# Performance work log

Hardware: AMD Instinct MI355X
Metric: run time of the kernel (lower is better)

Reference implementation:

```python
import jax, jax.numpy as jnp
import numpy as np

B, N, D_ROI = 16, 128, 12544   # images, detections/image, C*roi*roi = 256*7*7
HID, PARTS = 128, 22
DTH, CTH = 50.0, 0.8           # dist / cosine thresholds
EPS = 1e-12


def setup_inputs() -> dict:
    key = jax.random.key(0)
    ks = jax.random.split(key, 6)
    d_in = D_ROI + 2
    fv = jax.random.normal(ks[0], (B, N, D_ROI), jnp.float32)
    ctr = jax.random.uniform(ks[1], (B, N, 2), jnp.float32) * 640.0  # xyxyn*640 centers
    W1 = jax.random.normal(ks[2], (d_in, HID), jnp.float32) / np.float32(np.sqrt(d_in))
    b1 = jnp.zeros((HID,), jnp.float32)
    W2 = jax.random.normal(ks[3], (HID, HID), jnp.float32) / np.float32(np.sqrt(HID))
    b2 = jnp.zeros((HID,), jnp.float32)
    Wc = jax.random.normal(ks[4], (HID, PARTS), jnp.float32) / np.float32(np.sqrt(HID))
    bc = jnp.zeros((PARTS,), jnp.float32)
    return {"fv": fv, "ctr": ctr, "W1": W1, "b1": b1, "W2": W2, "b2": b2, "Wc": Wc, "bc": bc}


def _adjacency(fv, ctr):
    """Per-image graph build: (cdist < dth) | (cosine > cth), + PyG self-loop."""
    # squared pairwise distance (compare against DTH^2; avoids sqrt at 0)
    d2 = jnp.sum((ctr[:, :, None, :] - ctr[:, None, :, :]) ** 2, axis=-1)  # [B,N,N]
    fvn = fv / jnp.maximum(jnp.linalg.norm(fv, axis=-1, keepdims=True), EPS)
    cos = jnp.einsum("bnd,bmd->bnm", fvn, fvn)                              # [B,N,N]
    A = ((d2 < DTH * DTH) | (cos > CTH)).astype(jnp.float32)
    # GCNConv(add_self_loops=True) adds weight-1 self loops on top of existing edges
    A = A + jnp.eye(N, dtype=jnp.float32)
    deg = jnp.sum(A, axis=-1)                                               # >= 2 on diag
    dinv = jax.lax.rsqrt(deg)
    return dinv[:, :, None] * A * dinv[:, None, :]                          # D^-1/2 A D^-1/2


def reference(fv, ctr, W1, b1, W2, b2, Wc, bc):
    A_hat = _adjacency(fv, ctr)                         # [B,N,N]
    x = jnp.concatenate([fv, ctr], axis=-1)             # [B,N,D_roi+2]
    h = jax.nn.relu(jnp.einsum("bnm,bmh->bnh", A_hat, x @ W1) + b1)
    h = jax.nn.relu(jnp.einsum("bnm,bmh->bnh", A_hat, h @ W2) + b2)
    hg = jnp.mean(h, axis=1)                            # global_mean_pool per image
    logits = hg @ Wc + bc                               # [B, PARTS]
    return logits
```

## Files before the change

kernel.cpp:

```cpp
#include <hip/hip_runtime.h>
#include <stdint.h>

#define DROI   12544
#define BIMG   16
#define NDET   128
#define NHID   128

typedef __bf16 bf16x8 __attribute__((ext_vector_type(8)));
typedef float  f32x4  __attribute__((ext_vector_type(4)));

__device__ __forceinline__ unsigned pk2(float a, float b){
  unsigned ua = __float_as_uint(a), ub = __float_as_uint(b);
  ua = (ua + 0x7fffu + ((ua >> 16) & 1u)) >> 16;
  ub = (ub + 0x7fffu + ((ub >> 16) & 1u)) >> 16;
  return ua | (ub << 16);
}
__device__ __forceinline__ unsigned short bf1(float a){
  unsigned ua = __float_as_uint(a);
  return (unsigned short)((ua + 0x7fffu + ((ua >> 16) & 1u)) >> 16);
}
__device__ __forceinline__ f32x4 mfma16(bf16x8 a, bf16x8 b, f32x4 c){
  return __builtin_amdgcn_mfma_f32_16x16x32_bf16(a, b, c, 0, 0, 0);
}
__device__ __forceinline__ void gl_lds16(const void* g, void* l){
  __builtin_amdgcn_global_load_lds(
      (const __attribute__((address_space(1))) unsigned int*)g,
      (__attribute__((address_space(3))) unsigned int*)l, 16, 0, 0);
}
__device__ __forceinline__ bf16x8 ldfrag128(const short* base, int row, int bo){
  const char* p = (const char*)base + row * 128 + (bo ^ ((row & 7) << 4));
  return *(const bf16x8*)p;
}
__device__ __forceinline__ bf16x8 ldfrag256(const short* base, int row, int bo){
  const char* p = (const char*)base + row * 256 + (bo ^ ((row & 7) << 4));
  return *(const bf16x8*)p;
}

__global__ __launch_bounds__(256) void k0_wt(const float* __restrict__ W1,
                                             unsigned short* __restrict__ Wt){
  __shared__ float tile[64][133];
  const int t  = threadIdx.x;
  const int k0 = blockIdx.x * 64;
  const int r0 = t >> 5;
  const int c4 = (t & 31) * 4;
#pragma unroll
  for (int i = 0; i < 8; ++i){
    int r = r0 + i * 8;
    float4 v = *(const float4*)(W1 + (long)(k0 + r) * NHID + c4);
    tile[r][c4+0] = v.x; tile[r][c4+1] = v.y; tile[r][c4+2] = v.z; tile[r][c4+3] = v.w;
  }
  __syncthreads();
  const int h  = t >> 1;
  const int kc = (t & 1) * 32;
  unsigned* dst = (unsigned*)(Wt + (long)h * DROI + k0 + kc);
#pragma unroll
  for (int kk = 0; kk < 32; kk += 2)
    dst[kk >> 1] = pk2(tile[kc + kk][h], tile[kc + kk + 1][h]);
}

template<int SK>
__global__ __launch_bounds__(512, 4) void k1_main(const float* __restrict__ fv,
    const unsigned short* __restrict__ Wt, unsigned* __restrict__ part){
  constexpr int KC = DROI / SK;
  constexpr int NT = KC / 64;
  static_assert(NT >= 3, "pipeline needs >=3 tiles");
  __shared__ __align__(16) short lsA[2][8192];
  __shared__ __align__(16) short lsB[3][8192];
  const int tid  = threadIdx.x;
  const int wave = tid >> 6, lane = tid & 63;

  const int nwg  = SK * BIMG;
  const int cpx  = nwg >> 3;
  const int orig = blockIdx.x;
  const int wg   = (orig & 7) * cpx + (orig >> 3);
  const int s = wg >> 4;
  const int b = wg & 15;
  const int kbase = s * KC;

  f32x4 acc[2][8];
  {
    f32x4 z = {0.f, 0.f, 0.f, 0.f};
#pragma unroll
    for (int m = 0; m < 2; ++m)
#pragma unroll
      for (int c = 0; c < 8; ++c) acc[m][c] = z;
  }

  const int r0   = tid >> 2;
  const int colf = (tid & 3) * 4;
  const int sw   = (r0 & 7) << 4;
  const float* fvt = fv + (long)(b * NDET + r0) * DROI + kbase + colf;
  const int hh  = lane >> 3;
  const int seg = (lane & 7) ^ hh;

  const int outw = wave >> 2;
  const int mq   = wave & 3;
  const int lq   = lane & 15;

  float4 stg[4];

  auto issueF = [&](int t){
    const float* fp = fvt + t * 64;
#pragma unroll
    for (int i = 0; i < 4; ++i) stg[i] = *(const float4*)(fp + i * 16);
  };
  auto issueG = [&](int t, int bufi){
#pragma unroll
    for (int j = 0; j < 2; ++j){
      int call = wave * 2 + j;
      int h = call * 8 + hh;
      const char* g = (const char*)Wt + (long)h * (DROI * 2)
                    + (long)(kbase + t * 64) * 2 + seg * 16;
      gl_lds16(g, (char*)lsB[bufi] + call * 1024);
    }
  };
  auto writeA = [&](int abuf){
    char* basep = (char*)lsA[abuf];
#pragma unroll
    for (int i = 0; i < 4; ++i){
      uint2 w; w.x = pk2(stg[i].x, stg[i].y); w.y = pk2(stg[i].z, stg[i].w);
      int bo = (colf + i * 16) * 2;
      *(uint2*)(basep + r0 * 128 + (bo ^ sw)) = w;
    }
  };

  issueF(0);
  __builtin_amdgcn_sched_barrier(0);
  issueG(0, 0);
  issueG(1, 1);
  __builtin_amdgcn_sched_barrier(0);
  writeA(0);
  asm volatile("s_waitcnt vmcnt(2)" ::: "memory");
  asm volatile("s_waitcnt lgkmcnt(0)" ::: "memory");
  __builtin_amdgcn_sched_barrier(0);
  __builtin_amdgcn_s_barrier();
  __builtin_amdgcn_sched_barrier(0);

#pragma unroll
  for (int t = 0; t < NT; ++t){
    if (t + 1 < NT) issueF(t + 1);
    __builtin_amdgcn_sched_barrier(0);
    if (t + 2 < NT) issueG(t + 2, (t + 2) % 3);
    __builtin_amdgcn_sched_barrier(0);
    {
      const short* A  = lsA[t & 1];
      const short* Bs = outw ? lsB[t % 3] : lsA[t & 1];
#pragma unroll
      for (int kk = 0; kk < 2; ++kk){
        const int bo = kk * 64 + (lane >> 4) * 16;
        bf16x8 a0 = ldfrag128(A, mq * 32 + lq, bo);
        bf16x8 a1 = ldfrag128(A, mq * 32 + 16 + lq, bo);
#pragma unroll
        for (int cb = 0; cb < 8; ++cb){
          bf16x8 bb = ldfrag128(Bs, cb * 16 + lq, bo);
          acc[0][cb] = mfma16(a0, bb, acc[0][cb]);
          acc[1][cb] = mfma16(a1, bb, acc[1][cb]);
        }
      }
    }
    __builtin_amdgcn_sched_barrier(0);
    if (t + 1 < NT){
      writeA((t + 1) & 1);
      asm volatile("s_waitcnt lgkmcnt(0)" ::: "memory");
      __builtin_amdgcn_sched_barrier(0);
      __builtin_amdgcn_s_barrier();
      __builtin_amdgcn_sched_barrier(0);
    }
  }

  const int slot = mq * 64 + lane;
  uint4* dst4 = (uint4*)(part + (((long)s * 32 + b * 2 + outw) * 8192));
#pragma unroll
  for (int g = 0; g < 8; ++g){
    const int m = g >> 2, cb0 = (g & 3) * 2;
    uint4 w;
    w.x = pk2(acc[m][cb0][0],     acc[m][cb0][1]);
    w.y = pk2(acc[m][cb0][2],     acc[m][cb0][3]);
    w.z = pk2(acc[m][cb0 + 1][0], acc[m][cb0 + 1][1]);
    w.w = pk2(acc[m][cb0 + 1][2], acc[m][cb0 + 1][3]);
    dst4[g * 256 + slot] = w;
  }
}

template<int SK>
__global__ __launch_bounds__(256) void k_reduce(const unsigned* __restrict__ part,
                                                float* __restrict__ fin){
  __shared__ float tile[16][33];
  const int tid = threadIdx.x;
  const int B   = blockIdx.x;
  const int bo2 = B >> 5;
  const int q   = (B & 31) * 256 + tid;
  float lo = 0.f, hi = 0.f;
  const unsigned* p = part + (long)bo2 * 8192 + q;
#pragma unroll
  for (int s = 0; s < SK; ++s){
    unsigned v = p[(long)s * 262144];
    lo += __uint_as_float(v << 16);
    hi += __uint_as_float(v & 0xffff0000u);
  }
  const int g    = q >> 10;
  const int slot = (q & 1023) >> 2;
  const int w    = q & 3;
  const int m  = g >> 2;
  const int cb1 = w >> 1;
  const int ip = w & 1;
  const int mq = slot >> 6, lane = slot & 63;
  const int r   = ((lane >> 4) << 2) + (ip << 1);
  const int col = (cb1 << 4) + (lane & 15);
  tile[r][col]     = lo;
  tile[r + 1][col] = hi;
  __syncthreads();
  const int Rbase = mq * 32 + m * 16;
  const int Cbase = (g & 3) * 32;
  float* f = fin + (long)bo2 * 16384;
  if ((bo2 & 1) == 0){
#pragma unroll
    for (int k = 0; k < 2; ++k){
      int idx = k * 256 + tid;
      int rr = idx >> 5, cc = idx & 31;
      f[(Rbase + rr) * 128 + Cbase + cc] = tile[rr][cc];
    }
  } else {
#pragma unroll
    for (int k = 0; k < 2; ++k){
      int idx = k * 256 + tid;
      int cc = idx >> 4, rr = idx & 15;
      f[(Cbase + cc) * 128 + Rbase + rr] = tile[rr][cc];
    }
  }
}

__global__ __launch_bounds__(512, 1) void k2f(const float* __restrict__ fin,
    const float* __restrict__ ctr, const float* __restrict__ W1,
    const float* __restrict__ b1, const float* __restrict__ W2,
    const float* __restrict__ b2, const float* __restrict__ Wc,
    const float* __restrict__ bc, float* __restrict__ out){
  __shared__ __align__(16) short Ah[16384];
  __shared__ __align__(16) short Bu[16384];
  __shared__ __align__(16) short Cu[16384];
  __shared__ float sm2[256];
  __shared__ float sctr[256];
  const int b   = blockIdx.x;
  const int tid = threadIdx.x;
  const float* G  = fin + (long)b * 32768;
  const float* Yt = G + 16384;

  if (tid < 256) sctr[tid] = ctr[b * 256 + tid];
  if (tid < 128){
    float g = G[tid * 129];
    sm2[tid] = 1.0f / fmaxf(sqrtf(g), 1e-12f);
  }
  __syncthreads();

  const int   i   = tid >> 2;
  const int   jq  = (tid & 3) * 32;
  const float invni = sm2[i];
  const float cxi = sctr[2 * i], cyi = sctr[2 * i + 1];
  unsigned m0 = 0;
  int degloc = 0;
  for (int j4 = 0; j4 < 32; j4 += 4){
    float4 g4 = *(const float4*)(G + i * 128 + jq + j4);
    float gg[4] = {g4.x, g4.y, g4.z, g4.w};
#pragma unroll
    for (int u = 0; u < 4; ++u){
      int j = jq + j4 + u;
      float cs = gg[u] * invni * sm2[j];
      float dx = cxi - sctr[2 * j];
      float dy = cyi - sctr[2 * j + 1];
      float d2 = dx * dx + dy * dy;
      if (d2 < 2500.0f || cs > 0.8f){
        m0 |= (1u << (j4 + u));
        ++degloc;
      }
    }
  }
  if (i >= jq && i < jq + 32) ++degloc;
  degloc += __shfl_xor(degloc, 1);
  degloc += __shfl_xor(degloc, 2);
  if ((tid & 3) == 0) sm2[128 + i] = rsqrtf((float)degloc);
  __syncthreads();

  {
    const float dinvi = sm2[128 + i];
    char* AhB = (char*)Ah;
#pragma unroll
    for (int jp = 0; jp < 32; jp += 2){
      int j0 = jq + jp, j1 = j0 + 1;
      float a0 = ((m0 >> jp)       & 1u) ? 1.f : 0.f;
      float a1 = ((m0 >> (jp + 1)) & 1u) ? 1.f : 0.f;
      if (i == j0) a0 += 1.f;
      if (i == j1) a1 += 1.f;
      float v0 = dinvi * a0 * sm2[128 + j0];
      float v1 = dinvi * a1 * sm2[128 + j1];
      int bo = j0 * 2;
      *(unsigned*)(AhB + i * 256 + (bo ^ ((i & 7) << 4))) = pk2(v0, v1);
    }
  }

  {
    const int c  = tid & 127;
    const int kq = (tid >> 7) * 32;
    char* WB = (char*)Cu;
#pragma unroll
    for (int k8 = kq; k8 < kq + 32; k8 += 8){
      float f[8];
#pragma unroll
      for (int u = 0; u < 8; ++u) f[u] = W2[(k8 + u) * 128 + c];
      uint4 w;
      w.x = pk2(f[0], f[1]); w.y = pk2(f[2], f[3]);
      w.z = pk2(f[4], f[5]); w.w = pk2(f[6], f[7]);
      int bo = k8 * 2;
      *(uint4*)(WB + c * 256 + (bo ^ ((c & 7) << 4))) = w;
    }
  }
  {
    const int cr = tid >> 2;
    const int kq = (tid & 3) * 32;
    const float w1a = W1[(long)12544 * NHID + cr];
    const float w1b = W1[(long)12545 * NHID + cr];
    const float* Yr = Yt + cr * 128 + kq;
    char* YtB = (char*)Bu;
#pragma unroll
    for (int k8 = 0; k8 < 32; k8 += 8){
      float4 va = *(const float4*)(Yr + k8);
      float4 vb = *(const float4*)(Yr + k8 + 4);
      float f[8] = {va.x, va.y, va.z, va.w, vb.x, vb.y, vb.z, vb.w};
#pragma unroll
      for (int u = 0; u < 8; ++u){
        int k = kq + k8 + u;
        f[u] += sctr[2 * k] * w1a + sctr[2 * k + 1] * w1b;
      }
      uint4 w;
      w.x = pk2(f[0], f[1]); w.y = pk2(f[2], f[3]);
      w.z = pk2(f[4], f[5]); w.w = pk2(f[6], f[7]);
      int bo = (kq + k8) * 2;
      *(uint4*)(YtB + cr * 256 + (bo ^ ((cr & 7) << 4))) = w;
    }
  }
  __syncthreads();

  const int wave = tid >> 6, lane = tid & 63;
  const int lq = lane & 15;
  f32x4 acc[8];
  f32x4 z4 = {0.f, 0.f, 0.f, 0.f};

#pragma unroll
  for (int cc = 0; cc < 8; ++cc) acc[cc] = z4;
#pragma unroll
  for (int ks = 0; ks < 4; ++ks){
    const int bo = ks * 64 + (lane >> 4) * 16;
    bf16x8 a0 = ldfrag256(Ah, wave * 16 + lq, bo);
#pragma unroll
    for (int cb = 0; cb < 8; ++cb){
      bf16x8 bb = ldfrag256(Bu, cb * 16 + lq, bo);
      acc[cb] = mfma16(a0, bb, acc[cb]);
    }
  }
  __syncthreads();
  {
    char* BuB = (char*)Bu;
    const int R0 = wave * 16 + (lane >> 4) * 4;
#pragma unroll
    for (int cb = 0; cb < 8; ++cb){
      const int C = cb * 16 + lq;
      const float bb1 = b1[C];
#pragma unroll
      for (int u = 0; u < 4; ++u){
        float v = fmaxf(acc[cb][u] + bb1, 0.f);
        int row = R0 + u;
        *(unsigned short*)(BuB + row * 256 + ((C * 2) ^ ((row & 7) << 4))) = bf1(v);
      }
    }
  }
  __syncthreads();

#pragma unroll
  for (int cc = 0; cc < 8; ++cc) acc[cc] = z4;
#pragma unroll
  for (int ks = 0; ks < 4; ++ks){
    const int bo = ks * 64 + (lane >> 4) * 16;
    bf16x8 a0 = ldfrag256(Bu, wave * 16 + lq, bo);
#pragma unroll
    for (int cb = 0; cb < 8; ++cb){
      bf16x8 bb = ldfrag256(Cu, cb * 16 + lq, bo);
      acc[cb] = mfma16(a0, bb, acc[cb]);
    }
  }
  __syncthreads();
  {
    char* BuB = (char*)Bu;
    const int R0 = wave * 16 + (lane >> 4) * 4;
#pragma unroll
    for (int cb = 0; cb < 8; ++cb){
      const int C = cb * 16 + lq;
#pragma unroll
      for (int u = 0; u < 4; u += 2){
        int k = R0 + u;
        unsigned w = pk2(acc[cb][u], acc[cb][u + 1]);
        *(unsigned*)(BuB + C * 256 + ((k * 2) ^ ((C & 7) << 4))) = w;
      }
    }
  }
  __syncthreads();

#pragma unroll
  for (int cc = 0; cc < 8; ++cc) acc[cc] = z4;
#pragma unroll
  for (int ks = 0; ks < 4; ++ks){
    const int bo = ks * 64 + (lane >> 4) * 16;
    bf16x8 a0 = ldfrag256(Ah, wave * 16 + lq, bo);
#pragma unroll
    for (int cb = 0; cb < 8; ++cb){
      bf16x8 bb = ldfrag256(Bu, cb * 16 + lq, bo);
      acc[cb] = mfma16(a0, bb, acc[cb]);
    }
  }
  float colp[8];
#pragma unroll
  for (int cb = 0; cb < 8; ++cb){
    const float bb2 = b2[cb * 16 + lq];
    float sum = 0.f;
#pragma unroll
    for (int u = 0; u < 4; ++u)
      sum += fmaxf(acc[cb][u] + bb2, 0.f);
    colp[cb] = sum;
  }
#pragma unroll
  for (int cb = 0; cb < 8; ++cb){
    float v = colp[cb];
    v += __shfl_xor(v, 16);
    v += __shfl_xor(v, 32);
    colp[cb] = v;
  }
  float* hgp = (float*)Cu;
  if ((lane >> 4) == 0){
#pragma unroll
    for (int cb = 0; cb < 8; ++cb)
      hgp[wave * 128 + cb * 16 + lane] = colp[cb];
  }
  __syncthreads();
  float* hg = hgp + 1024;
  if (tid < 128){
    float s = 0.f;
#pragma unroll
    for (int w = 0; w < 8; ++w) s += hgp[w * 128 + tid];
    hg[tid] = s * (1.0f / 128.0f);
  }
  __syncthreads();
  if (tid < 22){
    float a2 = bc[tid];
    for (int h = 0; h < 128; ++h) a2 += hg[h] * Wc[h * 22 + tid];
    out[b * 22 + tid] = a2;
  }
}

extern "C" void kernel_launch(void* const* d_in, const int* in_sizes, int n_in,
                              void* d_out, int out_size, void* d_ws, size_t ws_size,
                              hipStream_t stream){
  (void)in_sizes; (void)n_in; (void)out_size;
  const float* fv  = (const float*)d_in[0];
  const float* ctr = (const float*)d_in[1];
  const float* W1  = (const float*)d_in[2];
  const float* b1  = (const float*)d_in[3];
  const float* W2  = (const float*)d_in[4];
  const float* b2  = (const float*)d_in[5];
  const float* Wc  = (const float*)d_in[6];
  const float* bc  = (const float*)d_in[7];
  char* ws = (char*)d_ws;
  float* out = (float*)d_out;

  const unsigned long SZ_WT  = (unsigned long)NHID * DROI * 2;
  const unsigned long SZ_FIN = (unsigned long)BIMG * 2 * 16384 * 4;

  const unsigned long need28 = SZ_WT + 28UL * 1048576UL + SZ_FIN;
  const bool big = (ws_size >= need28);
  const int SK = big ? 28 : 14;

  unsigned short* Wt   = (unsigned short*)(ws);
  unsigned*       part = (unsigned*)(ws + SZ_WT);
  float*          fin  = (float*)(ws + SZ_WT + (unsigned long)SK * 1048576UL);

  k0_wt<<<dim3(DROI / 64), dim3(256), 0, stream>>>(W1, Wt);
  if (big){
    k1_main<28><<<dim3(28 * BIMG), dim3(512), 0, stream>>>(fv, Wt, part);
    k_reduce<28><<<dim3(1024), dim3(256), 0, stream>>>(part, fin);
  } else {
    k1_main<14><<<dim3(14 * BIMG), dim3(512), 0, stream>>>(fv, Wt, part);
    k_reduce<14><<<dim3(1024), dim3(256), 0, stream>>>(part, fin);
  }
  k2f<<<dim3(BIMG), dim3(512), 0, stream>>>(fin, ctr, W1, b1, W2, b2, Wc, bc, out);
}
```

Measured before the change: 58.84 us.

## Load W1 fragments directly from global memory instead of staging through LDS

Removes the triple-buffered LDS staging of the transposed bf16 W1 tiles, which were filled with global_load_lds. The waves computing the x·W1 product now read their B fragments straight from global memory (served by L2/cache) inside the MFMA loop. This drops LDS usage and the vmcnt waits tied to the async copies, which may raise occupancy. The cost is that global load latency now sits directly in front of the MFMAs with no prefetch, and the loop branches by wave.

```diff
diff --git a/kernel.cpp b/kernel.cpp
--- a/kernel.cpp
+++ b/kernel.cpp
@@ -21,11 +21,6 @@
 }
 __device__ __forceinline__ f32x4 mfma16(bf16x8 a, bf16x8 b, f32x4 c){
   return __builtin_amdgcn_mfma_f32_16x16x32_bf16(a, b, c, 0, 0, 0);
-}
-__device__ __forceinline__ void gl_lds16(const void* g, void* l){
-  __builtin_amdgcn_global_load_lds(
-      (const __attribute__((address_space(1))) unsigned int*)g,
-      (__attribute__((address_space(3))) unsigned int*)l, 16, 0, 0);
 }
 __device__ __forceinline__ bf16x8 ldfrag128(const short* base, int row, int bo){
   const char* p = (const char*)base + row * 128 + (bo ^ ((row & 7) << 4));
@@ -63,9 +58,8 @@
     const unsigned short* __restrict__ Wt, unsigned* __restrict__ part){
   constexpr int KC = DROI / SK;
   constexpr int NT = KC / 64;
-  static_assert(NT >= 3, "pipeline needs >=3 tiles");
+  static_assert(NT >= 2, "need >=2 tiles");
   __shared__ __align__(16) short lsA[2][8192];
-  __shared__ __align__(16) short lsB[3][8192];
   const int tid  = threadIdx.x;
   const int wave = tid >> 6, lane = tid & 63;
 
@@ -90,29 +84,19 @@
   const int colf = (tid & 3) * 4;
   const int sw   = (r0 & 7) << 4;
   const float* fvt = fv + (long)(b * NDET + r0) * DROI + kbase + colf;
-  const int hh  = lane >> 3;
-  const int seg = (lane & 7) ^ hh;
 
   const int outw = wave >> 2;
   const int mq   = wave & 3;
   const int lq   = lane & 15;
 
+  const unsigned short* wtb = Wt + (long)lq * DROI + kbase + (lane >> 4) * 8;
+
   float4 stg[4];
 
   auto issueF = [&](int t){
     const float* fp = fvt + t * 64;
 #pragma unroll
     for (int i = 0; i < 4; ++i) stg[i] = *(const float4*)(fp + i * 16);
-  };
-  auto issueG = [&](int t, int bufi){
-#pragma unroll
-    for (int j = 0; j < 2; ++j){
-      int call = wave * 2 + j;
-      int h = call * 8 + hh;
-      const char* g = (const char*)Wt + (long)h * (DROI * 2)
-                    + (long)(kbase + t * 64) * 2 + seg * 16;
-      gl_lds16(g, (char*)lsB[bufi] + call * 1024);
-    }
   };
   auto writeA = [&](int abuf){
     char* basep = (char*)lsA[abuf];
@@ -126,11 +110,7 @@
 
   issueF(0);
   __builtin_amdgcn_sched_barrier(0);
-  issueG(0, 0);
-  issueG(1, 1);
-  __builtin_amdgcn_sched_barrier(0);
   writeA(0);
-  asm volatile("s_waitcnt vmcnt(2)" ::: "memory");
   asm volatile("s_waitcnt lgkmcnt(0)" ::: "memory");
   __builtin_amdgcn_sched_barrier(0);
   __builtin_amdgcn_s_barrier();
@@ -140,21 +120,34 @@
   for (int t = 0; t < NT; ++t){
     if (t + 1 < NT) issueF(t + 1);
     __builtin_amdgcn_sched_barrier(0);
-    if (t + 2 < NT) issueG(t + 2, (t + 2) % 3);
-    __builtin_amdgcn_sched_barrier(0);
     {
-      const short* A  = lsA[t & 1];
-      const short* Bs = outw ? lsB[t % 3] : lsA[t & 1];
-#pragma unroll
-      for (int kk = 0; kk < 2; ++kk){
-        const int bo = kk * 64 + (lane >> 4) * 16;
-        bf16x8 a0 = ldfrag128(A, mq * 32 + lq, bo);
-        bf16x8 a1 = ldfrag128(A, mq * 32 + 16 + lq, bo);
-#pragma unroll
-        for (int cb = 0; cb < 8; ++cb){
-          bf16x8 bb = ldfrag128(Bs, cb * 16 + lq, bo);
-          acc[0][cb] = mfma16(a0, bb, acc[0][cb]);
-          acc[1][cb] = mfma16(a1, bb, acc[1][cb]);
+      const short* A = lsA[t & 1];
+      if (outw == 0){
+#pragma unroll
+        for (int kk = 0; kk < 2; ++kk){
+          const int bo = kk * 64 + (lane >> 4) * 16;
+          bf16x8 a0 = ldfrag128(A, mq * 32 + lq, bo);
+          bf16x8 a1 = ldfrag128(A, mq * 32 + 16 + lq, bo);
+#pragma unroll
+          for (int cb = 0; cb < 8; ++cb){
+            bf16x8 bb = ldfrag128(A, cb * 16 + lq, bo);
+            acc[0][cb] = mfma16(a0, bb, acc[0][cb]);
+            acc[1][cb] = mfma16(a1, bb, acc[1][cb]);
+          }
+        }
+      } else {
+#pragma unroll
+        for (int kk = 0; kk < 2; ++kk){
+          const int bo = kk * 64 + (lane >> 4) * 16;
+          bf16x8 a0 = ldfrag128(A, mq * 32 + lq, bo);
+          bf16x8 a1 = ldfrag128(A, mq * 32 + 16 + lq, bo);
+          const unsigned short* wp = wtb + t * 64 + kk * 32;
+#pragma unroll
+          for (int cb = 0; cb < 8; ++cb){
+            bf16x8 bb = *(const bf16x8*)(wp + (long)cb * 16 * DROI);
+            acc[0][cb] = mfma16(a0, bb, acc[0][cb]);
+            acc[1][cb] = mfma16(a1, bb, acc[1][cb]);
+          }
         }
       }
     }
```

After: 120.1 us. 104% more time.

## Retile wave MFMA blocks to 64x64 and shrink B pipeline to double buffer

Applied to the files above, without the earlier changes.

Changes each wave's output tile from 32x128 to a 64x64 square, so every B fragment is reused across four A fragments. This cuts LDS fragment reads per MFMA. The W loads now come only from the four waves that consume lsB, and the B ring drops from triple to double buffering with prefetch distance one, freeing LDS. The shorter prefetch distance may expose more global latency, and the reduce kernel's index mapping is updated to match the new accumulator layout.

```diff
diff --git a/kernel.cpp b/kernel.cpp
--- a/kernel.cpp
+++ b/kernel.cpp
@@ -63,9 +63,9 @@
     const unsigned short* __restrict__ Wt, unsigned* __restrict__ part){
   constexpr int KC = DROI / SK;
   constexpr int NT = KC / 64;
-  static_assert(NT >= 3, "pipeline needs >=3 tiles");
+  static_assert(NT >= 2, "need >=2 tiles");
   __shared__ __align__(16) short lsA[2][8192];
-  __shared__ __align__(16) short lsB[3][8192];
+  __shared__ __align__(16) short lsB[2][8192];
   const int tid  = threadIdx.x;
   const int wave = tid >> 6, lane = tid & 63;
 
@@ -77,13 +77,13 @@
   const int b = wg & 15;
   const int kbase = s * KC;
 
-  f32x4 acc[2][8];
+  f32x4 acc[4][4];
   {
     f32x4 z = {0.f, 0.f, 0.f, 0.f};
 #pragma unroll
-    for (int m = 0; m < 2; ++m)
-#pragma unroll
-      for (int c = 0; c < 8; ++c) acc[m][c] = z;
+    for (int m = 0; m < 4; ++m)
+#pragma unroll
+      for (int c = 0; c < 4; ++c) acc[m][c] = z;
   }
 
   const int r0   = tid >> 2;
@@ -94,25 +94,29 @@
   const int seg = (lane & 7) ^ hh;
 
   const int outw = wave >> 2;
-  const int mq   = wave & 3;
+  const int wq   = wave & 3;
+  const int wr   = wq & 1;
+  const int wc   = wq >> 1;
   const int lq   = lane & 15;
 
   float4 stg[4];
 
+  auto issueG = [&](int t, int bufi){
+    if (outw == 1){
+#pragma unroll
+      for (int j = 0; j < 4; ++j){
+        int call = wq * 4 + j;
+        int h = call * 8 + hh;
+        const char* g = (const char*)Wt + (long)h * (DROI * 2)
+                      + (long)(kbase + t * 64) * 2 + seg * 16;
+        gl_lds16(g, (char*)lsB[bufi] + call * 1024);
+      }
+    }
+  };
   auto issueF = [&](int t){
     const float* fp = fvt + t * 64;
 #pragma unroll
     for (int i = 0; i < 4; ++i) stg[i] = *(const float4*)(fp + i * 16);
-  };
-  auto issueG = [&](int t, int bufi){
-#pragma unroll
-    for (int j = 0; j < 2; ++j){
-      int call = wave * 2 + j;
-      int h = call * 8 + hh;
-      const char* g = (const char*)Wt + (long)h * (DROI * 2)
-                    + (long)(kbase + t * 64) * 2 + seg * 16;
-      gl_lds16(g, (char*)lsB[bufi] + call * 1024);
-    }
   };
   auto writeA = [&](int abuf){
     char* basep = (char*)lsA[abuf];
@@ -124,13 +128,11 @@
     }
   };
 
+  issueG(0, 0);
+  __builtin_amdgcn_sched_barrier(0);
   issueF(0);
   __builtin_amdgcn_sched_barrier(0);
-  issueG(0, 0);
-  issueG(1, 1);
-  __builtin_amdgcn_sched_barrier(0);
   writeA(0);
-  asm volatile("s_waitcnt vmcnt(2)" ::: "memory");
   asm volatile("s_waitcnt lgkmcnt(0)" ::: "memory");
   __builtin_amdgcn_sched_barrier(0);
   __builtin_amdgcn_s_barrier();
@@ -138,23 +140,28 @@
 
 #pragma unroll
   for (int t = 0; t < NT; ++t){
-    if (t + 1 < NT) issueF(t + 1);
-    __builtin_amdgcn_sched_barrier(0);
-    if (t + 2 < NT) issueG(t + 2, (t + 2) % 3);
-    __builtin_amdgcn_sched_barrier(0);
+    if (t + 1 < NT){
+      issueG(t + 1, (t + 1) & 1);
+      __builtin_amdgcn_sched_barrier(0);
+      issueF(t + 1);
+      __builtin_amdgcn_sched_barrier(0);
+    }
     {
       const short* A  = lsA[t & 1];
-      const short* Bs = outw ? lsB[t % 3] : lsA[t & 1];
+      const short* Bs = outw ? (const short*)lsB[t & 1] : A;
 #pragma unroll
       for (int kk = 0; kk < 2; ++kk){
         const int bo = kk * 64 + (lane >> 4) * 16;
-        bf16x8 a0 = ldfrag128(A, mq * 32 + lq, bo);
-        bf16x8 a1 = ldfrag128(A, mq * 32 + 16 + lq, bo);
-#pragma unroll
-        for (int cb = 0; cb < 8; ++cb){
-          bf16x8 bb = ldfrag128(Bs, cb * 16 + lq, bo);
-          acc[0][cb] = mfma16(a0, bb, acc[0][cb]);
-          acc[1][cb] = mfma16(a1, bb, acc[1][cb]);
+        bf16x8 am[4];
+#pragma unroll
+        for (int m = 0; m < 4; ++m)
+          am[m] = ldfrag128(A, wr * 64 + m * 16 + lq, bo);
+#pragma unroll
+        for (int cb = 0; cb < 4; ++cb){
+          bf16x8 bb = ldfrag128(Bs, wc * 64 + cb * 16 + lq, bo);
+#pragma unroll
+          for (int m = 0; m < 4; ++m)
+            acc[m][cb] = mfma16(am[m], bb, acc[m][cb]);
         }
       }
     }
@@ -168,11 +175,11 @@
     }
   }
 
-  const int slot = mq * 64 + lane;
+  const int slot = wq * 64 + lane;
   uint4* dst4 = (uint4*)(part + (((long)s * 32 + b * 2 + outw) * 8192));
 #pragma unroll
   for (int g = 0; g < 8; ++g){
-    const int m = g >> 2, cb0 = (g & 3) * 2;
+    const int m = g >> 1, cb0 = (g & 1) * 2;
     uint4 w;
     w.x = pk2(acc[m][cb0][0],     acc[m][cb0][1]);
     w.y = pk2(acc[m][cb0][2],     acc[m][cb0][3]);
@@ -200,18 +207,19 @@
   }
   const int g    = q >> 10;
   const int slot = (q & 1023) >> 2;
-  const int w    = q & 3;
-  const int m  = g >> 2;
-  const int cb1 = w >> 1;
-  const int ip = w & 1;
-  const int mq = slot >> 6, lane = slot & 63;
-  const int r   = ((lane >> 4) << 2) + (ip << 1);
-  const int col = (cb1 << 4) + (lane & 15);
+  const int wb   = q & 3;
+  const int m    = g >> 1;
+  const int cbl  = wb >> 1;
+  const int ip   = wb & 1;
+  const int wq   = slot >> 6;
+  const int lane = slot & 63;
+  const int r    = ((lane >> 4) << 2) + (ip << 1);
+  const int col  = (cbl << 4) + (lane & 15);
   tile[r][col]     = lo;
   tile[r + 1][col] = hi;
   __syncthreads();
-  const int Rbase = mq * 32 + m * 16;
-  const int Cbase = (g & 3) * 32;
+  const int Rbase = (wq & 1) * 64 + m * 16;
+  const int Cbase = (wq >> 1) * 64 + (g & 1) * 32;
   float* f = fin + (long)bo2 * 16384;
   if ((bo2 & 1) == 0){
 #pragma unroll
```

Result: slower. 60.87 us (+3.5%).

## Warp-specialize main GEMM with dedicated producer waves and fixed split-K of 14

Applied to the files above, without the earlier changes.

The fused GEMM kernel becomes warp-specialized: 8 consumer waves run MFMAs while 2 extra producer waves load fv (converting it to bf16) and the transposed W1 tile into double-buffered LDS, with one block barrier per tile. The triple-buffered B ring and the interleaved per-wave prefetch are removed. Split-K is fixed at 14 instead of choosing 28 when the workspace allows, so there are fewer, longer blocks. The producer waves now carry all global loads through only two waves, which may limit memory bandwidth, and halving the grid reduces parallelism.

```diff
diff --git a/kernel.cpp b/kernel.cpp
--- a/kernel.cpp
+++ b/kernel.cpp
@@ -59,13 +59,13 @@
 }
 
 template<int SK>
-__global__ __launch_bounds__(512, 4) void k1_main(const float* __restrict__ fv,
+__global__ __launch_bounds__(640, 2) void k1_main(const float* __restrict__ fv,
     const unsigned short* __restrict__ Wt, unsigned* __restrict__ part){
   constexpr int KC = DROI / SK;
   constexpr int NT = KC / 64;
-  static_assert(NT >= 3, "pipeline needs >=3 tiles");
+  static_assert(NT >= 2, "need >=2 tiles");
   __shared__ __align__(16) short lsA[2][8192];
-  __shared__ __align__(16) short lsB[3][8192];
+  __shared__ __align__(16) short lsB[2][8192];
   const int tid  = threadIdx.x;
   const int wave = tid >> 6, lane = tid & 63;
 
@@ -77,74 +77,61 @@
   const int b = wg & 15;
   const int kbase = s * KC;
 
-  f32x4 acc[2][8];
-  {
-    f32x4 z = {0.f, 0.f, 0.f, 0.f};
-#pragma unroll
-    for (int m = 0; m < 2; ++m)
-#pragma unroll
-      for (int c = 0; c < 8; ++c) acc[m][c] = z;
-  }
-
-  const int r0   = tid >> 2;
-  const int colf = (tid & 3) * 4;
-  const int sw   = (r0 & 7) << 4;
-  const float* fvt = fv + (long)(b * NDET + r0) * DROI + kbase + colf;
   const int hh  = lane >> 3;
   const int seg = (lane & 7) ^ hh;
 
-  const int outw = wave >> 2;
-  const int mq   = wave & 3;
-  const int lq   = lane & 15;
-
-  float4 stg[4];
-
-  auto issueF = [&](int t){
-    const float* fp = fvt + t * 64;
-#pragma unroll
-    for (int i = 0; i < 4; ++i) stg[i] = *(const float4*)(fp + i * 16);
-  };
-  auto issueG = [&](int t, int bufi){
-#pragma unroll
-    for (int j = 0; j < 2; ++j){
-      int call = wave * 2 + j;
+  const int pt   = tid - 512;
+  const int prow = pt >> 4;
+  const int pcol = (pt & 15) * 4;
+  const int psw  = (prow & 7) << 4;
+  const float* fvp = fv + (long)(b * NDET + prow) * DROI + kbase + pcol;
+  const int pw = wave - 8;
+
+  auto produce = [&](int t, int bufi){
+#pragma unroll
+    for (int j = 0; j < 8; ++j){
+      int call = pw * 8 + j;
       int h = call * 8 + hh;
       const char* g = (const char*)Wt + (long)h * (DROI * 2)
                     + (long)(kbase + t * 64) * 2 + seg * 16;
       gl_lds16(g, (char*)lsB[bufi] + call * 1024);
     }
+    char* basep = (char*)lsA[bufi];
+    const float* fp = fvp + t * 64;
+#pragma unroll
+    for (int batch = 0; batch < 4; ++batch){
+      float4 v[4];
+#pragma unroll
+      for (int i = 0; i < 4; ++i)
+        v[i] = *(const float4*)(fp + (long)((batch * 4 + i) * 8) * DROI);
+#pragma unroll
+      for (int i = 0; i < 4; ++i){
+        int row = (batch * 4 + i) * 8 + prow;
+        uint2 w; w.x = pk2(v[i].x, v[i].y); w.y = pk2(v[i].z, v[i].w);
+        *(uint2*)(basep + row * 128 + ((pcol * 2) ^ psw)) = w;
+      }
+    }
   };
-  auto writeA = [&](int abuf){
-    char* basep = (char*)lsA[abuf];
-#pragma unroll
-    for (int i = 0; i < 4; ++i){
-      uint2 w; w.x = pk2(stg[i].x, stg[i].y); w.y = pk2(stg[i].z, stg[i].w);
-      int bo = (colf + i * 16) * 2;
-      *(uint2*)(basep + r0 * 128 + (bo ^ sw)) = w;
-    }
-  };
-
-  issueF(0);
-  __builtin_amdgcn_sched_barrier(0);
-  issueG(0, 0);
-  issueG(1, 1);
-  __builtin_amdgcn_sched_barrier(0);
-  writeA(0);
-  asm volatile("s_waitcnt vmcnt(2)" ::: "memory");
-  asm volatile("s_waitcnt lgkmcnt(0)" ::: "memory");
-  __builtin_amdgcn_sched_barrier(0);
-  __builtin_amdgcn_s_barrier();
-  __builtin_amdgcn_sched_barrier(0);
-
-#pragma unroll
+
+  const int outw = wave >> 2;
+  const int mq   = wave & 3;
+  const int lq   = lane & 15;
+  f32x4 acc[2][8];
+  {
+    f32x4 z = {0.f, 0.f, 0.f, 0.f};
+#pragma unroll
+    for (int m = 0; m < 2; ++m)
+#pragma unroll
+      for (int c = 0; c < 8; ++c) acc[m][c] = z;
+  }
+
+  if (wave >= 8) produce(0, 0);
+  __syncthreads();
+
   for (int t = 0; t < NT; ++t){
-    if (t + 1 < NT) issueF(t + 1);
-    __builtin_amdgcn_sched_barrier(0);
-    if (t + 2 < NT) issueG(t + 2, (t + 2) % 3);
-    __builtin_amdgcn_sched_barrier(0);
-    {
+    if (wave < 8){
       const short* A  = lsA[t & 1];
-      const short* Bs = outw ? lsB[t % 3] : lsA[t & 1];
+      const short* Bs = outw ? (const short*)lsB[t & 1] : A;
 #pragma unroll
       for (int kk = 0; kk < 2; ++kk){
         const int bo = kk * 64 + (lane >> 4) * 16;
@@ -157,28 +144,25 @@
           acc[1][cb] = mfma16(a1, bb, acc[1][cb]);
         }
       }
-    }
-    __builtin_amdgcn_sched_barrier(0);
-    if (t + 1 < NT){
-      writeA((t + 1) & 1);
-      asm volatile("s_waitcnt lgkmcnt(0)" ::: "memory");
-      __builtin_amdgcn_sched_barrier(0);
-      __builtin_amdgcn_s_barrier();
-      __builtin_amdgcn_sched_barrier(0);
-    }
-  }
-
-  const int slot = mq * 64 + lane;
-  uint4* dst4 = (uint4*)(part + (((long)s * 32 + b * 2 + outw) * 8192));
-#pragma unroll
-  for (int g = 0; g < 8; ++g){
-    const int m = g >> 2, cb0 = (g & 3) * 2;
-    uint4 w;
-    w.x = pk2(acc[m][cb0][0],     acc[m][cb0][1]);
-    w.y = pk2(acc[m][cb0][2],     acc[m][cb0][3]);
-    w.z = pk2(acc[m][cb0 + 1][0], acc[m][cb0 + 1][1]);
-    w.w = pk2(acc[m][cb0 + 1][2], acc[m][cb0 + 1][3]);
-    dst4[g * 256 + slot] = w;
+    } else if (t + 1 < NT){
+      produce(t + 1, (t + 1) & 1);
+    }
+    __syncthreads();
+  }
+
+  if (wave < 8){
+    const int slot = mq * 64 + lane;
+    uint4* dst4 = (uint4*)(part + (((long)s * 32 + b * 2 + outw) * 8192));
+#pragma unroll
+    for (int g = 0; g < 8; ++g){
+      const int m = g >> 2, cb0 = (g & 3) * 2;
+      uint4 w;
+      w.x = pk2(acc[m][cb0][0],     acc[m][cb0][1]);
+      w.y = pk2(acc[m][cb0][2],     acc[m][cb0][3]);
+      w.z = pk2(acc[m][cb0 + 1][0], acc[m][cb0 + 1][1]);
+      w.w = pk2(acc[m][cb0 + 1][2], acc[m][cb0 + 1][3]);
+      dst4[g * 256 + slot] = w;
+    }
   }
 }
 
@@ -457,7 +441,7 @@
 extern "C" void kernel_launch(void* const* d_in, const int* in_sizes, int n_in,
                               void* d_out, int out_size, void* d_ws, size_t ws_size,
                               hipStream_t stream){
-  (void)in_sizes; (void)n_in; (void)out_size;
+  (void)in_sizes; (void)n_in; (void)out_size; (void)ws_size;
   const float* fv  = (const float*)d_in[0];
   const float* ctr = (const float*)d_in[1];
   const float* W1  = (const float*)d_in[2];
@@ -469,24 +453,14 @@
   char* ws = (char*)d_ws;
   float* out = (float*)d_out;
 
-  const unsigned long SZ_WT  = (unsigned long)NHID * DROI * 2;
-  const unsigned long SZ_FIN = (unsigned long)BIMG * 2 * 16384 * 4;
-
-  const unsigned long need28 = SZ_WT + 28UL * 1048576UL + SZ_FIN;
-  const bool big = (ws_size >= need28);
-  const int SK = big ? 28 : 14;
+  const unsigned long SZ_WT = (unsigned long)NHID * DROI * 2;
 
   unsigned short* Wt   = (unsigned short*)(ws);
   unsigned*       part = (unsigned*)(ws + SZ_WT);
-  float*          fin  = (float*)(ws + SZ_WT + (unsigned long)SK * 1048576UL);
+  float*          fin  = (float*)(ws + SZ_WT + 14UL * 1048576UL);
 
   k0_wt<<<dim3(DROI / 64), dim3(256), 0, stream>>>(W1, Wt);
-  if (big){
-    k1_main<28><<<dim3(28 * BIMG), dim3(512), 0, stream>>>(fv, Wt, part);
-    k_reduce<28><<<dim3(1024), dim3(256), 0, stream>>>(part, fin);
-  } else {
-    k1_main<14><<<dim3(14 * BIMG), dim3(512), 0, stream>>>(fv, Wt, part);
-    k_reduce<14><<<dim3(1024), dim3(256), 0, stream>>>(part, fin);
-  }
+  k1_main<14><<<dim3(14 * BIMG), dim3(640), 0, stream>>>(fv, Wt, part);
+  k_reduce<14><<<dim3(1024), dim3(256), 0, stream>>>(part, fin);
   k2f<<<dim3(BIMG), dim3(512), 0, stream>>>(fin, ctr, W1, b1, W2, b2, Wc, bc, out);
 }
```

Result: slower. 111.8 us (+90.1%).
